# Kernel optimization log

Measured on AMD Instinct MI355X. Metric: run time of the kernel, lower is better.

Reference implementation:

```python
import jax, jax.numpy as jnp
import numpy as np

RADIUS = 5
WIN = (RADIUS - 1) * 2 + 1  # 9


def setup_inputs() -> dict:
    key = jax.random.key(0)
    k1, k2 = jax.random.split(key)
    B, K, H, W = 4, 4, 224, 224
    seg = jax.random.uniform(k1, (B, K, H, W), dtype=jnp.float32)
    weight = jax.random.uniform(k2, (B, 1, H, W, WIN, WIN), dtype=jnp.float32)
    return {"seg": seg, "weight": weight}


def reference(seg, weight):
    # seg: [B,K,H,W]; weight: [B,1,H,W,w,w] local affinity window, w = 2*(radius-1)+1
    B, K, H, W = seg.shape
    Kconst = jnp.float32(K)
    # torch pads by `radius` on all sides but only uses window offsets 0..2*(radius-1),
    # i.e. relative offsets [-radius, radius-2] -- replicate exactly.
    padded = jnp.pad(seg, ((0, 0), (0, 0), (RADIUS, RADIUS), (RADIUS, RADIUS)))
    # weighted sum over the local window without materializing [B,K,H,W,w,w]
    sum_w_seg = jnp.zeros_like(seg)
    for m in range(WIN):
        for n in range(WIN):
            sum_w_seg = sum_w_seg + padded[:, :, m:m + H, n:n + W] * weight[:, :, :, :, m, n]
    assocA = jnp.sum(sum_w_seg * seg, axis=(-1, -2))                      # [B,K]
    assocV = jnp.sum(jnp.sum(weight, axis=(-1, -2)) * seg, axis=(-1, -2))  # [B,K]
    assoc = jnp.sum(assocA / assocV, axis=-1)                              # [B]
    return jnp.sum(Kconst - assoc)
```

## Files before the change

### kernel.cpp

```cpp
#include <hip/hip_runtime.h>

#define RADIUS 5
#define WIN 9
#define BB 4
#define KK 4
#define HH 224
#define WW 224
#define HW (HH * WW)
#define PD 234
#define PAREA (PD * PD)
#define NBUCKET 64
#define PARTIAL_FLOATS (NBUCKET * BB * 8)
#define ELEMS_PER_B (HW * 81)
#define STEPS 28
#define WAVE_ELEMS (64 * STEPS)
#define BLOCK_WAVES 4
#define BLOCK_ELEMS (BLOCK_WAVES * WAVE_ELEMS)
#define BLOCKS_PER_B (ELEMS_PER_B / BLOCK_ELEMS)
#define TOTAL_BLOCKS (BB * BLOCKS_PER_B)


__global__ __launch_bounds__(256) void ncuts_pad(
    const float* __restrict__ seg, float4* __restrict__ pseg, float* __restrict__ zr)
{
    const int tid = blockIdx.x * 256 + threadIdx.x;
    if (tid < PARTIAL_FLOATS) zr[tid] = 0.f;
    if (tid >= BB * PAREA) return;
    const int b  = tid / PAREA;
    const int rc = tid - b * PAREA;
    const int r  = rc / PD;
    const int c  = rc - r * PD;
    const int hh = r - RADIUS;
    const int ww = c - RADIUS;
    float4 v = {0.f, 0.f, 0.f, 0.f};
    if (hh >= 0 && hh < HH && ww >= 0 && ww < WW) {
        const float* sb = seg + (size_t)b * KK * HW + hh * WW + ww;
        v.x = sb[0 * HW];
        v.y = sb[1 * HW];
        v.z = sb[2 * HW];
        v.w = sb[3 * HW];
    }
    pseg[tid] = v;
}

__global__ __launch_bounds__(256) void ncuts_main(
    const float* __restrict__ weight,
    const float4* __restrict__ pseg,
    float* __restrict__ partial)
{
    const int lane = threadIdx.x & 63;
    const int wid  = threadIdx.x >> 6;
    const int b    = blockIdx.x / BLOCKS_PER_B;
    const int blkb = blockIdx.x - b * BLOCKS_PER_B;

    const unsigned wave_base = (unsigned)(blkb * BLOCK_WAVES + wid) * WAVE_ELEMS;
    const unsigned idx0 = wave_base + (unsigned)lane;

    const float*  wsrc = weight + (size_t)b * ELEMS_PER_B;
    const float4* p4   = pseg   + (size_t)b * PAREA;

    unsigned p = idx0 / 81u;
    unsigned o = idx0 - p * 81u;
    unsigned h = p / 224u;
    unsigned w = p - h * 224u;

    float a0 = 0.f, a1 = 0.f, a2 = 0.f, a3 = 0.f;
    float v0 = 0.f, v1 = 0.f, v2 = 0.f, v3 = 0.f;

    #pragma unroll
    for (int j = 0; j < STEPS; ++j) {
        const float wv = wsrc[wave_base + j * 64 + lane];

        const unsigned m = o / 9u;
        const unsigned n = o - m * 9u;

        const float4 sc = p4[(h + RADIUS) * PD + (w + RADIUS)];
        const float4 sv = p4[(h + m) * PD + (w + n)];

        const float w0 = wv * sc.x;
        const float w1 = wv * sc.y;
        const float w2 = wv * sc.z;
        const float w3 = wv * sc.w;

        a0 = fmaf(w0, sv.x, a0);
        a1 = fmaf(w1, sv.y, a1);
        a2 = fmaf(w2, sv.z, a2);
        a3 = fmaf(w3, sv.w, a3);
        v0 += w0; v1 += w1; v2 += w2; v3 += w3;

        o += 64u;
        if (o >= 81u) {
            o -= 81u;
            ++w;
            if (w == 224u) { w = 0u; ++h; }
        }
    }

    float vals[8] = { a0, a1, a2, a3, v0, v1, v2, v3 };
    #pragma unroll
    for (int i = 0; i < 8; ++i) {
        float v = vals[i];
        v += __shfl_down(v, 32);
        v += __shfl_down(v, 16);
        v += __shfl_down(v, 8);
        v += __shfl_down(v, 4);
        v += __shfl_down(v, 2);
        v += __shfl_down(v, 1);
        vals[i] = v;
    }

    if (lane == 0) {
        const int bucket = (blkb + wid * 16) & (NBUCKET - 1);
        float* dst = partial + (bucket * BB + b) * 8;
        #pragma unroll
        for (int i = 0; i < 8; ++i)
            atomicAdd(dst + i, vals[i]);
    }
}

__global__ __launch_bounds__(64) void ncuts_final(
    const float* __restrict__ partial, float* __restrict__ out)
{
    __shared__ float sums[32];
    const int t = threadIdx.x;
    if (t < 32) {
        float s = 0.f;
        for (int bucket = 0; bucket < NBUCKET; ++bucket)
            s += partial[bucket * 32 + t];
        sums[t] = s;
    }
    __syncthreads();
    if (t == 0) {
        float total = 0.f;
        for (int b = 0; b < BB; ++b) {
            float assoc = 0.f;
            for (int k = 0; k < KK; ++k) {
                const float A = sums[b * 8 + k];
                const float V = sums[b * 8 + 4 + k];
                assoc += A / V;
            }
            total += (float)KK - assoc;
        }
        out[0] = total;
    }
}

extern "C" void kernel_launch(void* const* d_in, const int* in_sizes, int n_in,
                              void* d_out, int out_size, void* d_ws, size_t ws_size,
                              hipStream_t stream) {
    const float* seg    = (const float*)d_in[0];
    const float* weight = (const float*)d_in[1];
    float* out     = (float*)d_out;
    float* wsf     = (float*)d_ws;
    float* partial = wsf;
    float4* pseg   = (float4*)(wsf + PARTIAL_FLOATS);

    {
        const int total = BB * PAREA;
        const int grid  = (total + 255) / 256;
        hipLaunchKernelGGL(ncuts_pad, dim3(grid), dim3(256), 0, stream, seg, pseg, wsf);
    }

    hipLaunchKernelGGL(ncuts_main, dim3(TOTAL_BLOCKS), dim3(256), 0, stream,
                       weight, pseg, partial);

    hipLaunchKernelGGL(ncuts_final, dim3(1), dim3(64), 0, stream, partial, out);
}
```

Measured before the change: 114.8 us.

## Tile main kernel by row segments and stage padded seg rows in LDS

```diff
diff --git a/kernel.cpp b/kernel.cpp
--- a/kernel.cpp
+++ b/kernel.cpp
@@ -11,13 +11,14 @@
 #define PAREA (PD * PD)
 #define NBUCKET 64
 #define PARTIAL_FLOATS (NBUCKET * BB * 8)
-#define ELEMS_PER_B (HW * 81)
-#define STEPS 28
-#define WAVE_ELEMS (64 * STEPS)
-#define BLOCK_WAVES 4
-#define BLOCK_ELEMS (BLOCK_WAVES * WAVE_ELEMS)
-#define BLOCKS_PER_B (ELEMS_PER_B / BLOCK_ELEMS)
+
+#define TILE_PIX 56
+#define WT_PER_ROW 4
+#define BLOCKS_PER_B (HH * WT_PER_ROW)
 #define TOTAL_BLOCKS (BB * BLOCKS_PER_B)
+#define TILE_ELEMS (TILE_PIX * 81)
+#define NSTEPS 18
+#define TILE_COLS 64
 
 
 __global__ __launch_bounds__(256) void ncuts_pad(
@@ -48,52 +49,63 @@
     const float4* __restrict__ pseg,
     float* __restrict__ partial)
 {
-    const int lane = threadIdx.x & 63;
-    const int wid  = threadIdx.x >> 6;
-    const int b    = blockIdx.x / BLOCKS_PER_B;
-    const int blkb = blockIdx.x - b * BLOCKS_PER_B;
+    __shared__ float4 ptile[WIN * TILE_COLS];
 
-    const unsigned wave_base = (unsigned)(blkb * BLOCK_WAVES + wid) * WAVE_ELEMS;
-    const unsigned idx0 = wave_base + (unsigned)lane;
+    const int tid  = threadIdx.x;
+    const int lane = tid & 63;
+    const int wid  = tid >> 6;
+    const int blk  = blockIdx.x;
+    const int b    = blk / BLOCKS_PER_B;
+    const int rem  = blk - b * BLOCKS_PER_B;
+    const int h    = rem >> 2;
+    const int w0   = (rem & 3) * TILE_PIX;
 
-    const float*  wsrc = weight + (size_t)b * ELEMS_PER_B;
-    const float4* p4   = pseg   + (size_t)b * PAREA;
+    const float4* p4 = pseg + (size_t)b * PAREA;
+    {
+        const float4* src0 = p4 + h * PD + w0;
+        #pragma unroll
+        for (int rr = 0; rr < WIN; ++rr) {
+            if ((rr & 3) == wid)
+                __builtin_amdgcn_global_load_lds(
+                    (__attribute__((address_space(1))) void*)(src0 + rr * PD + lane),
+                    (__attribute__((address_space(3))) void*)(ptile + rr * TILE_COLS),
+                    16, 0, 0);
+        }
+    }
+    __syncthreads();
 
-    unsigned p = idx0 / 81u;
-    unsigned o = idx0 - p * 81u;
-    unsigned h = p / 224u;
-    unsigned w = p - h * 224u;
+    const float* wsrc = weight + ((size_t)b * HW + (size_t)h * WW + w0) * 81;
+
+    unsigned e = (unsigned)tid;
+    unsigned q = e / 81u;
+    unsigned o = e - q * 81u;
 
     float a0 = 0.f, a1 = 0.f, a2 = 0.f, a3 = 0.f;
     float v0 = 0.f, v1 = 0.f, v2 = 0.f, v3 = 0.f;
 
     #pragma unroll
-    for (int j = 0; j < STEPS; ++j) {
-        const float wv = wsrc[wave_base + j * 64 + lane];
+    for (int j = 0; j < NSTEPS; ++j) {
+        if (e < TILE_ELEMS) {
+            const float wv = wsrc[e];
+            const unsigned m = o / 9u;
+            const unsigned n = o - m * 9u;
 
-        const unsigned m = o / 9u;
-        const unsigned n = o - m * 9u;
+            const float4 sc = ptile[5 * TILE_COLS + q + 5];
+            const float4 sv = ptile[m * TILE_COLS + q + n];
 
-        const float4 sc = p4[(h + RADIUS) * PD + (w + RADIUS)];
-        const float4 sv = p4[(h + m) * PD + (w + n)];
-
-        const float w0 = wv * sc.x;
-        const float w1 = wv * sc.y;
-        const float w2 = wv * sc.z;
-        const float w3 = wv * sc.w;
-
-        a0 = fmaf(w0, sv.x, a0);
-        a1 = fmaf(w1, sv.y, a1);
-        a2 = fmaf(w2, sv.z, a2);
-        a3 = fmaf(w3, sv.w, a3);
-        v0 += w0; v1 += w1; v2 += w2; v3 += w3;
-
-        o += 64u;
-        if (o >= 81u) {
-            o -= 81u;
-            ++w;
-            if (w == 224u) { w = 0u; ++h; }
+            const float t0 = wv * sc.x;
+            const float t1 = wv * sc.y;
+            const float t2 = wv * sc.z;
+            const float t3 = wv * sc.w;
+            a0 = fmaf(t0, sv.x, a0);
+            a1 = fmaf(t1, sv.y, a1);
+            a2 = fmaf(t2, sv.z, a2);
+            a3 = fmaf(t3, sv.w, a3);
+            v0 += t0; v1 += t1; v2 += t2; v3 += t3;
         }
+        e += 256u;
+        o += 13u; q += 3u;
+        if (o >= 81u) { o -= 81u; ++q; }
     }
 
     float vals[8] = { a0, a1, a2, a3, v0, v1, v2, v3 };
@@ -108,9 +120,8 @@
         v += __shfl_down(v, 1);
         vals[i] = v;
     }
-
     if (lane == 0) {
-        const int bucket = (blkb + wid * 16) & (NBUCKET - 1);
+        const int bucket = ((blk << 2) | wid) & (NBUCKET - 1);
         float* dst = partial + (bucket * BB + b) * 8;
         #pragma unroll
         for (int i = 0; i < 8; ++i)
```

Result: slower. 120.6 us (+5.1%).
